# Kernel tuning notes

Hardware: AMD Instinct MI355X
Metric: run time of the kernel (lower is better)

## Reference

```python
import jax, jax.numpy as jnp
import numpy as np

N_NODES = 100000
N_EDGES = 1600000
IN_C, HID_C, OUT_C = 128, 128, 64


def gcn_conv(x, W, b, src, dst, n_nodes):
    """PyG-style GCNConv: h = x @ W; add self-loops; symmetric deg^-1/2 norm;
    scatter-add aggregation; + bias. Self-loop contribution added analytically
    (norm for self-loop edge i->i is deg_i^-1) instead of materializing edges."""
    h = x @ W  # [N, C_out]
    # degree over dst including self-loops (edge weights are all ones)
    deg = jax.ops.segment_sum(jnp.ones((src.shape[0],), h.dtype), dst,
                              num_segments=n_nodes) + 1.0
    dinv = jax.lax.rsqrt(deg)  # deg >= 1 always
    norm = dinv[src] * dinv[dst]  # [E]
    agg = jax.ops.segment_sum(h[src] * norm[:, None], dst, num_segments=n_nodes)
    agg = agg + h * (dinv * dinv)[:, None]  # self-loop term
    return agg + b


def setup_inputs() -> dict:
    key = jax.random.key(0)
    k0, k1, k2, k3, k4, k5 = jax.random.split(key, 6)
    x = jax.random.normal(k0, (N_NODES, IN_C), dtype=jnp.float32)
    edge_index = jax.random.randint(k1, (2, N_EDGES), 0, N_NODES, dtype=jnp.int64)
    s1 = 1.0 / np.sqrt(IN_C)
    s2 = 1.0 / np.sqrt(HID_C)
    W1 = jax.random.uniform(k2, (IN_C, HID_C), jnp.float32, -s1, s1)
    b1 = jax.random.uniform(k3, (HID_C,), jnp.float32, -s1, s1)
    W2 = jax.random.uniform(k4, (HID_C, OUT_C), jnp.float32, -s2, s2)
    b2 = jax.random.uniform(k5, (OUT_C,), jnp.float32, -s2, s2)
    return {"x": x, "W1": W1, "b1": b1, "W2": W2, "b2": b2,
            "edge_index": edge_index}


def reference(x, W1, b1, W2, b2, edge_index):
    src, dst = edge_index[0], edge_index[1]
    h = gcn_conv(x, W1, b1, src, dst, N_NODES)
    h = jax.nn.relu(h)
    out = gcn_conv(h, W2, b2, src, dst, N_NODES)
    return out
```

## Files before the change

### kernel.cpp

```cpp
#include <hip/hip_runtime.h>


static constexpr int BSHIFT = 7;
static constexpr int BWIDTH = 1 << BSHIFT;
static constexpr int MAXBUCK = 2048;
static constexpr int NPART = 256;

static constexpr size_t OFF_FLAG = 0;
static constexpr size_t OFF_DEG  = 256;
static constexpr size_t OFF_ROW  = 458752;
static constexpr size_t OFF_BSUM = 917504;
static constexpr size_t OFF_CCNT = 925696;
static constexpr size_t OFF_COFF = 937984;
static constexpr size_t OFF_DINV = 962560;
static constexpr size_t OFF_CSR  = 1376256;
static constexpr size_t OFF_HS1  = 8388608;
static constexpr size_t OFF_OUT1 = 35651584;
static constexpr size_t OFF_HS2  = 62914560;
static constexpr size_t OFF_H2   = 75714560;

__device__ __forceinline__ unsigned short f2bf(float f) {
    unsigned u = __float_as_uint(f);
    u += 0x7fffu + ((u >> 16) & 1u);
    return (unsigned short)(u >> 16);
}

typedef __attribute__((ext_vector_type(8))) short bf16x8;
typedef __attribute__((ext_vector_type(4))) float f32x4;
typedef __attribute__((ext_vector_type(4))) unsigned u32x4;

__global__ void detect_kernel(const unsigned* __restrict__ w,
                              unsigned* __restrict__ flag,
                              unsigned* __restrict__ ccnt, int nbuck) {
    int i = blockIdx.x * blockDim.x + threadIdx.x;
    if (i <= nbuck) ccnt[i] = 0;
    if (w[2 * i + 1] != 0u) atomicOr(flag, 1u);
}

__device__ __forceinline__ int edge_dst(const unsigned* w, unsigned flag,
                                        int e, int E) {
    return flag ? (int)w[E + e] : (int)w[2 * E + 2 * e];
}
__device__ __forceinline__ int edge_src(const unsigned* w, unsigned flag,
                                        int e, int E) {
    return flag ? (int)w[e] : (int)w[2 * e];
}

__global__ __launch_bounds__(1024) void coarse_hist_kernel(
    const unsigned* __restrict__ w, const unsigned* __restrict__ flag,
    unsigned* __restrict__ ccnt, unsigned* __restrict__ h2, int E, int nbuck) {
    __shared__ unsigned hist[MAXBUCK];
    for (int i = threadIdx.x; i < nbuck; i += 1024) hist[i] = 0;
    __syncthreads();
    const unsigned f = *flag;
    const int per = (E + gridDim.x - 1) / gridDim.x;
    const int e0 = blockIdx.x * per, e1 = min(E, e0 + per);
    for (int e = e0 + (int)threadIdx.x; e < e1; e += 1024)
        atomicAdd(&hist[edge_dst(w, f, e, E) >> BSHIFT], 1u);
    __syncthreads();
    for (int i = threadIdx.x; i < nbuck; i += 1024) {
        unsigned h = hist[i];
        h2[(size_t)i * NPART + blockIdx.x] = h;
        if (h) atomicAdd(&ccnt[i], h);
    }
}

__global__ __launch_bounds__(1024) void coarse_scan_kernel(
    const unsigned* __restrict__ ccnt, unsigned* __restrict__ coff, int nbuck) {
    __shared__ unsigned sh[1024];
    const int t = threadIdx.x;
    unsigned run = 0;
    for (int b0 = 0; b0 < nbuck; b0 += 1024) {
        unsigned v = (b0 + t < nbuck) ? ccnt[b0 + t] : 0u;
        sh[t] = v;
        __syncthreads();
        for (int off = 1; off < 1024; off <<= 1) {
            unsigned a = (t >= off) ? sh[t - off] : 0u;
            __syncthreads();
            sh[t] += a;
            __syncthreads();
        }
        if (b0 + t < nbuck) coff[b0 + t] = run + sh[t] - v;
        run += sh[1023];
        __syncthreads();
    }
    if (t == 0) coff[nbuck] = run;
}

__global__ __launch_bounds__(NPART) void off2d_kernel(
    unsigned* __restrict__ h2, const unsigned* __restrict__ coff) {
    __shared__ unsigned sh[NPART];
    const int b = blockIdx.x, t = threadIdx.x;
    unsigned v = h2[(size_t)b * NPART + t];
    sh[t] = v;
    __syncthreads();
#pragma unroll
    for (int off = 1; off < NPART; off <<= 1) {
        unsigned a = (t >= off) ? sh[t - off] : 0u;
        __syncthreads();
        sh[t] += a;
        __syncthreads();
    }
    h2[(size_t)b * NPART + t] = coff[b] + sh[t] - v;
}

__global__ __launch_bounds__(1024) void partition_kernel(
    const unsigned* __restrict__ w, const unsigned* __restrict__ flag,
    const unsigned* __restrict__ h2, unsigned* __restrict__ part, int E,
    int nbuck) {
    __shared__ unsigned lcur[MAXBUCK];
    for (int i = threadIdx.x; i < nbuck; i += 1024)
        lcur[i] = h2[(size_t)i * NPART + blockIdx.x];
    __syncthreads();
    const unsigned f = *flag;
    const int per = (E + gridDim.x - 1) / gridDim.x;
    const int e0 = blockIdx.x * per, e1 = min(E, e0 + per);
    for (int e = e0 + (int)threadIdx.x; e < e1; e += 1024) {
        int d = edge_dst(w, f, e, E);
        int s = edge_src(w, f, e, E);
        unsigned pos = atomicAdd(&lcur[d >> BSHIFT], 1u);
        part[pos] = (unsigned)s | ((unsigned)(d & (BWIDTH - 1)) << 20);
    }
}

__global__ __launch_bounds__(256) void bucket_csr_kernel(
    const unsigned* __restrict__ part, const unsigned* __restrict__ coff,
    unsigned* __restrict__ deg, int* __restrict__ csr, int N) {
    __shared__ unsigned cnt[BWIDTH];
    __shared__ unsigned sc[BWIDTH];
    __shared__ unsigned cur[BWIDTH];
    const int b = blockIdx.x, base = b << BSHIFT, t = threadIdx.x;
    if (t < BWIDTH) cnt[t] = 0;
    __syncthreads();
    const int e0 = (int)coff[b], e1 = (int)coff[b + 1];
    for (int e = e0 + t; e < e1; e += 256)
        atomicAdd(&cnt[part[e] >> 20], 1u);
    __syncthreads();
    if (t < BWIDTH && base + t < N) deg[base + t] = cnt[t];
    if (t < BWIDTH) sc[t] = cnt[t];
    __syncthreads();
#pragma unroll
    for (int off = 1; off < BWIDTH; off <<= 1) {
        unsigned a = (t < BWIDTH && t >= off) ? sc[t - off] : 0u;
        __syncthreads();
        if (t < BWIDTH) sc[t] += a;
        __syncthreads();
    }
    if (t < BWIDTH) cur[t] = (unsigned)e0 + sc[t] - cnt[t];
    __syncthreads();
    for (int e = e0 + t; e < e1; e += 256) {
        unsigned pk = part[e];
        unsigned p = atomicAdd(&cur[pk >> 20], 1u);
        csr[p] = (int)(pk & 0xFFFFFu);
    }
}

__global__ __launch_bounds__(1024) void scan1_kernel(
    const unsigned* __restrict__ deg, unsigned* __restrict__ row,
    unsigned* __restrict__ bsum, int N) {
    __shared__ unsigned sh[1024];
    int gid = blockIdx.x * 1024 + threadIdx.x;
    int t = threadIdx.x;
    unsigned v = (gid < N) ? deg[gid] : 0u;
    sh[t] = v;
    __syncthreads();
#pragma unroll
    for (int off = 1; off < 1024; off <<= 1) {
        unsigned add = (t >= off) ? sh[t - off] : 0u;
        __syncthreads();
        sh[t] += add;
        __syncthreads();
    }
    if (gid < N) row[gid + 1] = sh[t];
    if (t == 1023) bsum[blockIdx.x] = sh[1023];
}

__global__ __launch_bounds__(1024) void scan2_kernel(unsigned* __restrict__ bsum,
                                                     int NB) {
    __shared__ unsigned sh[1024];
    const int t = threadIdx.x;
    unsigned v = (t < NB) ? bsum[t] : 0u;
    sh[t] = v;
    __syncthreads();
#pragma unroll
    for (int off = 1; off < 1024; off <<= 1) {
        unsigned a = (t >= off) ? sh[t - off] : 0u;
        __syncthreads();
        sh[t] += a;
        __syncthreads();
    }
    if (t < NB) bsum[t] = sh[t] - v;
}

__global__ void scan3_kernel(unsigned* __restrict__ row,
                             const unsigned* __restrict__ bsum,
                             const unsigned* __restrict__ deg,
                             float* __restrict__ dinv, int N) {
    int gid = blockIdx.x * blockDim.x + threadIdx.x;
    if (gid >= N) return;
    row[gid + 1] += bsum[gid >> 10];
    if (gid == 0) row[0] = 0u;
    dinv[gid] = rsqrtf((float)deg[gid] + 1.0f);
}

template <int BN, bool ABF16>
__global__ __launch_bounds__(256) void gemm_mfma(
    const void* __restrict__ Av, const float* __restrict__ B,
    const float* __restrict__ dinv, unsigned short* __restrict__ out, int M) {
    constexpr int NT = BN / 16;
    __shared__ short sA[16384];
    __shared__ short sB[NT * 2048];

    const int t = threadIdx.x;
    const int row0 = blockIdx.x * 128;
    const int w = t >> 6, lane = t & 63;
    const int m = lane & 15, q = lane >> 4;

    if (ABF16) {
        const unsigned short* A = (const unsigned short*)Av;
        for (int g = t; g < 2048; g += 256) {
            int r = g >> 4, k0 = (g & 15) << 3;
            uint4 v = make_uint4(0u, 0u, 0u, 0u);
            if (row0 + r < M) v = *(const uint4*)(A + (size_t)(row0 + r) * 128 + k0);
            int off = ((((r >> 4) * 4 + (k0 >> 5)) * 16 + (r & 15)) * 4 +
                       ((k0 >> 3) & 3)) * 8;
            *(uint4*)(sA + off) = v;
        }
    } else {
        const float* A = (const float*)Av;
        for (int g = t; g < 4096; g += 256) {
            int r = g >> 5, k0 = (g & 31) << 2;
            float4 v = make_float4(0.f, 0.f, 0.f, 0.f);
            if (row0 + r < M) v = *(const float4*)(A + (size_t)(row0 + r) * 128 + k0);
            ushort4 u;
            u.x = f2bf(v.x); u.y = f2bf(v.y); u.z = f2bf(v.z); u.w = f2bf(v.w);
            int off = ((((r >> 4) * 4 + (k0 >> 5)) * 16 + (r & 15)) * 4 +
                       ((k0 >> 3) & 3)) * 8 + (k0 & 4);
            *(ushort4*)(sA + off) = u;
        }
    }
    for (int g = t; g < BN * 32; g += 256) {
        int n = g % BN, k0 = (g / BN) * 4;
        float f0 = B[(size_t)(k0 + 0) * BN + n];
        float f1 = B[(size_t)(k0 + 1) * BN + n];
        float f2 = B[(size_t)(k0 + 2) * BN + n];
        float f3 = B[(size_t)(k0 + 3) * BN + n];
        ushort4 u;
        u.x = f2bf(f0); u.y = f2bf(f1); u.z = f2bf(f2); u.w = f2bf(f3);
        int off = ((((n >> 4) * 4 + (k0 >> 5)) * 16 + (n & 15)) * 4 +
                   ((k0 >> 3) & 3)) * 8 + (k0 & 4);
        *(ushort4*)(sB + off) = u;
    }
    __syncthreads();

    f32x4 acc[2][NT];
#pragma unroll
    for (int lt = 0; lt < 2; lt++)
#pragma unroll
        for (int nt = 0; nt < NT; nt++) acc[lt][nt] = (f32x4){0.f, 0.f, 0.f, 0.f};

    const int fb = (m * 4 + q) * 8;
#pragma unroll
    for (int ks = 0; ks < 4; ks++) {
        bf16x8 a0 = *(const bf16x8*)(sA + ((w * 2 + 0) * 4 + ks) * 512 + fb);
        bf16x8 a1 = *(const bf16x8*)(sA + ((w * 2 + 1) * 4 + ks) * 512 + fb);
#pragma unroll
        for (int nt = 0; nt < NT; nt++) {
            bf16x8 b = *(const bf16x8*)(sB + (nt * 4 + ks) * 512 + fb);
            acc[0][nt] = __builtin_amdgcn_mfma_f32_16x16x32_bf16(a0, b, acc[0][nt], 0, 0, 0);
            acc[1][nt] = __builtin_amdgcn_mfma_f32_16x16x32_bf16(a1, b, acc[1][nt], 0, 0, 0);
        }
    }

#pragma unroll
    for (int lt = 0; lt < 2; lt++) {
#pragma unroll
        for (int r = 0; r < 4; r++) {
            int row = row0 + w * 32 + lt * 16 + q * 4 + r;
            if (row < M) {
                float s = dinv[row];
#pragma unroll
                for (int nt = 0; nt < NT; nt++)
                    out[(size_t)row * BN + nt * 16 + m] = f2bf(acc[lt][nt][r] * s);
            }
        }
    }
}

#define ACC8(u)                                                                \
    do {                                                                       \
        s0 += __uint_as_float((u).x << 16);                                    \
        s1 += __uint_as_float((u).x & 0xffff0000u);                            \
        s2 += __uint_as_float((u).y << 16);                                    \
        s3 += __uint_as_float((u).y & 0xffff0000u);                            \
        s4 += __uint_as_float((u).z << 16);                                    \
        s5 += __uint_as_float((u).z & 0xffff0000u);                            \
        s6 += __uint_as_float((u).w << 16);                                    \
        s7 += __uint_as_float((u).w & 0xffff0000u);                            \
    } while (0)

template <int C, bool RELU, bool OUTBF>
__global__ __launch_bounds__(256) void agg_kernel(
    const int* __restrict__ csr, const unsigned* __restrict__ row,
    const unsigned short* __restrict__ hsb, const float* __restrict__ dinv,
    const float* __restrict__ bias, void* __restrict__ outv, int N) {
    constexpr int LPN = C / 8;
    const int tid = blockIdx.x * 256 + threadIdx.x;
    const int i = tid / LPN;
    const int l = tid % LPN;
    if (i >= N) return;

    const int co = 8 * l;
    const unsigned short* __restrict__ tab = hsb + co;
    float s0 = 0.f, s1 = 0.f, s2 = 0.f, s3 = 0.f,
          s4 = 0.f, s5 = 0.f, s6 = 0.f, s7 = 0.f;
    {
        uint4 u = *(const uint4*)(tab + (size_t)i * C);
        ACC8(u);
    }

    const int rs = (int)row[i], re = (int)row[i + 1];
    int e = rs;
    int idx = (rs + l < re) ? csr[rs + l] : 0;
    while (e < re) {
        const int cnt = min(LPN, re - e);
        const int idx_c = idx;
        e += LPN;
        idx = (e + l < re) ? csr[e + l] : 0;
        if (cnt == LPN) {
#pragma unroll
            for (int h = 0; h < LPN / 8; ++h) {
                uint4 v[8];
#pragma unroll
                for (int j = 0; j < 8; ++j) {
                    const int s = __shfl(idx_c, h * 8 + j, LPN);
                    v[j] = *(const uint4*)(tab + (size_t)s * C);
                }
#pragma unroll
                for (int j = 0; j < 8; ++j) ACC8(v[j]);
            }
        } else {
            for (int j = 0; j < cnt; ++j) {
                const int s = __shfl(idx_c, j, LPN);
                uint4 v = *(const uint4*)(tab + (size_t)s * C);
                ACC8(v);
            }
        }
    }

    const float sc = dinv[i];
    const float4 ba = *(const float4*)(bias + co);
    const float4 bb = *(const float4*)(bias + co + 4);
    float o0 = s0 * sc + ba.x, o1 = s1 * sc + ba.y;
    float o2 = s2 * sc + ba.z, o3 = s3 * sc + ba.w;
    float o4 = s4 * sc + bb.x, o5 = s5 * sc + bb.y;
    float o6 = s6 * sc + bb.z, o7 = s7 * sc + bb.w;
    if (RELU) {
        o0 = fmaxf(o0, 0.f); o1 = fmaxf(o1, 0.f); o2 = fmaxf(o2, 0.f);
        o3 = fmaxf(o3, 0.f); o4 = fmaxf(o4, 0.f); o5 = fmaxf(o5, 0.f);
        o6 = fmaxf(o6, 0.f); o7 = fmaxf(o7, 0.f);
    }
    if (OUTBF) {
        u32x4 u;
        u.x = (unsigned)f2bf(o0) | ((unsigned)f2bf(o1) << 16);
        u.y = (unsigned)f2bf(o2) | ((unsigned)f2bf(o3) << 16);
        u.z = (unsigned)f2bf(o4) | ((unsigned)f2bf(o5) << 16);
        u.w = (unsigned)f2bf(o6) | ((unsigned)f2bf(o7) << 16);
        __builtin_nontemporal_store(
            u, (u32x4*)((unsigned short*)outv + (size_t)i * C + co));
    } else {
        f32x4 a = (f32x4){o0, o1, o2, o3};
        f32x4 b = (f32x4){o4, o5, o6, o7};
        float* op = (float*)outv + (size_t)i * C + co;
        __builtin_nontemporal_store(a, (f32x4*)op);
        __builtin_nontemporal_store(b, (f32x4*)(op + 4));
    }
}

extern "C" void kernel_launch(void* const* d_in, const int* in_sizes, int n_in,
                              void* d_out, int out_size, void* d_ws,
                              size_t ws_size, hipStream_t stream) {
    const float* x  = (const float*)d_in[0];
    const float* W1 = (const float*)d_in[1];
    const float* b1 = (const float*)d_in[2];
    const float* W2 = (const float*)d_in[3];
    const float* b2 = (const float*)d_in[4];
    const unsigned* ew = (const unsigned*)d_in[5];
    const int E = in_sizes[5] / 2;
    const int N = in_sizes[0] / 128;
    const int NB = (N + 1023) >> 10;
    const int nbuck = (N + BWIDTH - 1) >> BSHIFT;

    char* ws = (char*)d_ws;
    unsigned* flag = (unsigned*)(ws + OFF_FLAG);
    unsigned* deg  = (unsigned*)(ws + OFF_DEG);
    unsigned* row  = (unsigned*)(ws + OFF_ROW);
    unsigned* bsum = (unsigned*)(ws + OFF_BSUM);
    unsigned* ccnt = (unsigned*)(ws + OFF_CCNT);
    unsigned* coff = (unsigned*)(ws + OFF_COFF);
    float* dinv    = (float*)(ws + OFF_DINV);
    int* csr       = (int*)(ws + OFF_CSR);
    unsigned short* hs1  = (unsigned short*)(ws + OFF_HS1);
    unsigned short* out1 = (unsigned short*)(ws + OFF_OUT1);
    unsigned short* hs2  = (unsigned short*)(ws + OFF_HS2);
    unsigned* h2   = (unsigned*)(ws + OFF_H2);
    unsigned* part = (unsigned*)(ws + OFF_HS1);

    hipMemsetAsync(flag, 0, 4, stream);

    detect_kernel<<<16, 256, 0, stream>>>(ew, flag, ccnt, nbuck);
    coarse_hist_kernel<<<NPART, 1024, 0, stream>>>(ew, flag, ccnt, h2, E, nbuck);
    coarse_scan_kernel<<<1, 1024, 0, stream>>>(ccnt, coff, nbuck);
    off2d_kernel<<<nbuck, NPART, 0, stream>>>(h2, coff);
    partition_kernel<<<NPART, 1024, 0, stream>>>(ew, flag, h2, part, E, nbuck);
    bucket_csr_kernel<<<nbuck, 256, 0, stream>>>(part, coff, deg, csr, N);
    scan1_kernel<<<NB, 1024, 0, stream>>>(deg, row, bsum, N);
    scan2_kernel<<<1, 1024, 0, stream>>>(bsum, NB);
    scan3_kernel<<<(N + 255) / 256, 256, 0, stream>>>(row, bsum, deg, dinv, N);

    gemm_mfma<128, false><<<(N + 127) / 128, 256, 0, stream>>>(x, W1, dinv, hs1, N);
    agg_kernel<128, true, true><<<(N * 16 + 255) / 256, 256, 0, stream>>>(
        csr, row, hs1, dinv, b1, out1, N);

    gemm_mfma<64, true><<<(N + 127) / 128, 256, 0, stream>>>(out1, W2, dinv, hs2, N);
    agg_kernel<64, false, false><<<(N * 8 + 255) / 256, 256, 0, stream>>>(
        csr, row, hs2, dinv, b2, d_out, N);
}
```

Measured before the change: 328.5 us.

## Store GEMM output in 16-column slices and aggregate per slice for L2 locality

The GEMM epilogue now writes the bf16 feature table as column slices of 16 channels, each slice contiguous over all nodes. The aggregation kernel is restructured so each block handles one slice for 128 nodes, with two lanes per node. Block indices are interleaved across slices so each slice's working set (N×32 bytes) can stay in cache while random gathers hit it. Index and row-pointer loads become nontemporal. The cost is that csr and row are re-read once per slice, and the per-edge loop is less unrolled, leaving fewer loads in flight.

```diff
diff --git a/kernel.cpp b/kernel.cpp
--- a/kernel.cpp
+++ b/kernel.cpp
@@ -281,7 +281,7 @@
                 float s = dinv[row];
 #pragma unroll
                 for (int nt = 0; nt < NT; nt++)
-                    out[(size_t)row * BN + nt * 16 + m] = f2bf(acc[lt][nt][r] * s);
+                    out[((size_t)nt * M + row) * 16 + m] = f2bf(acc[lt][nt][r] * s);
             }
         }
     }
@@ -299,55 +299,56 @@
         s7 += __uint_as_float((u).w & 0xffff0000u);                            \
     } while (0)
 
-template <int C, bool RELU, bool OUTBF>
-__global__ __launch_bounds__(256) void agg_kernel(
+template <int C, int NSLICE, bool RELU, bool OUTBF>
+__global__ __launch_bounds__(256) void agg_sliced(
     const int* __restrict__ csr, const unsigned* __restrict__ row,
     const unsigned short* __restrict__ hsb, const float* __restrict__ dinv,
     const float* __restrict__ bias, void* __restrict__ outv, int N) {
-    constexpr int LPN = C / 8;
-    const int tid = blockIdx.x * 256 + threadIdx.x;
-    const int i = tid / LPN;
-    const int l = tid % LPN;
+    const int r8 = blockIdx.x & 7;
+    int slice, chunk;
+    if (NSLICE == 8) {
+        slice = r8;
+        chunk = blockIdx.x >> 3;
+    } else {
+        slice = r8 & 3;
+        chunk = ((blockIdx.x >> 3) << 1) | (r8 >> 2);
+    }
+    const int i = chunk * 128 + ((int)threadIdx.x >> 1);
+    const int l = threadIdx.x & 1;
     if (i >= N) return;
 
-    const int co = 8 * l;
-    const unsigned short* __restrict__ tab = hsb + co;
+    const unsigned short* __restrict__ tab =
+        hsb + (size_t)slice * N * 16 + 8 * l;
+
     float s0 = 0.f, s1 = 0.f, s2 = 0.f, s3 = 0.f,
           s4 = 0.f, s5 = 0.f, s6 = 0.f, s7 = 0.f;
     {
-        uint4 u = *(const uint4*)(tab + (size_t)i * C);
+        uint4 u = *(const uint4*)(tab + (size_t)i * 16);
         ACC8(u);
     }
 
-    const int rs = (int)row[i], re = (int)row[i + 1];
+    const int rs = (int)__builtin_nontemporal_load(row + i);
+    const int re = (int)__builtin_nontemporal_load(row + i + 1);
     int e = rs;
-    int idx = (rs + l < re) ? csr[rs + l] : 0;
+    int nxt = (e + l < re) ? __builtin_nontemporal_load(csr + e + l) : 0;
     while (e < re) {
-        const int cnt = min(LPN, re - e);
-        const int idx_c = idx;
-        e += LPN;
-        idx = (e + l < re) ? csr[e + l] : 0;
-        if (cnt == LPN) {
-#pragma unroll
-            for (int h = 0; h < LPN / 8; ++h) {
-                uint4 v[8];
-#pragma unroll
-                for (int j = 0; j < 8; ++j) {
-                    const int s = __shfl(idx_c, h * 8 + j, LPN);
-                    v[j] = *(const uint4*)(tab + (size_t)s * C);
-                }
-#pragma unroll
-                for (int j = 0; j < 8; ++j) ACC8(v[j]);
-            }
+        const int cur = nxt;
+        const int cnt = re - e;
+        e += 2;
+        nxt = (e + l < re) ? __builtin_nontemporal_load(csr + e + l) : 0;
+        const int sa = __shfl(cur, 0, 2);
+        uint4 va = *(const uint4*)(tab + (size_t)sa * 16);
+        if (cnt >= 2) {
+            const int sb = __shfl(cur, 1, 2);
+            uint4 vb = *(const uint4*)(tab + (size_t)sb * 16);
+            ACC8(va);
+            ACC8(vb);
         } else {
-            for (int j = 0; j < cnt; ++j) {
-                const int s = __shfl(idx_c, j, LPN);
-                uint4 v = *(const uint4*)(tab + (size_t)s * C);
-                ACC8(v);
-            }
-        }
-    }
-
+            ACC8(va);
+        }
+    }
+
+    const int co = slice * 16 + 8 * l;
     const float sc = dinv[i];
     const float4 ba = *(const float4*)(bias + co);
     const float4 bb = *(const float4*)(bias + co + 4);
@@ -418,11 +419,14 @@
     scan2_kernel<<<1, 1024, 0, stream>>>(bsum, NB);
     scan3_kernel<<<(N + 255) / 256, 256, 0, stream>>>(row, bsum, deg, dinv, N);
 
+    const int chunks = (N + 127) / 128;
+    const int pairs  = (chunks + 1) / 2;
+
     gemm_mfma<128, false><<<(N + 127) / 128, 256, 0, stream>>>(x, W1, dinv, hs1, N);
-    agg_kernel<128, true, true><<<(N * 16 + 255) / 256, 256, 0, stream>>>(
+    agg_sliced<128, 8, true, true><<<chunks * 8, 256, 0, stream>>>(
         csr, row, hs1, dinv, b1, out1, N);
 
     gemm_mfma<64, true><<<(N + 127) / 128, 256, 0, stream>>>(out1, W2, dinv, hs2, N);
-    agg_kernel<64, false, false><<<(N * 8 + 255) / 256, 256, 0, stream>>>(
+    agg_sliced<64, 4, false, false><<<pairs * 8, 256, 0, stream>>>(
         csr, row, hs2, dinv, b2, d_out, N);
 }
```

Result: slower. 471.4 us (+43.5%).
